# Performance work log

Hardware: AMD Instinct MI355X
Metric: run time of the kernel (lower is better)

The kernel has to match this reference:

```python
import jax, jax.numpy as jnp
import numpy as np

MAX_POINTS = 32
EPS = 1e-5


def setup_inputs() -> dict:
    key = jax.random.key(0)
    k1, k2, k3, k4, k5, k6 = jax.random.split(key, 6)
    M, P, C_IN, C_OUT = 40000, MAX_POINTS, 4, 64
    voxel_features = jax.random.normal(k1, (M, P, C_IN), dtype=jnp.float32)
    voxel_num_points = jax.random.randint(k2, (M,), 0, MAX_POINTS, dtype=jnp.int32)
    # Linear(C_in, C_out) params (PyTorch default init scale ~ U(-1/sqrt(fan_in), ...))
    lim = 1.0 / np.sqrt(C_IN)
    W = jax.random.uniform(k3, (C_OUT, C_IN), minval=-lim, maxval=lim, dtype=jnp.float32)
    b = jax.random.uniform(k4, (C_OUT,), minval=-lim, maxval=lim, dtype=jnp.float32)
    # BatchNorm1d affine params
    gamma = jnp.ones((C_OUT,), dtype=jnp.float32)
    beta = jnp.zeros((C_OUT,), dtype=jnp.float32)
    return {"voxel_features": voxel_features, "voxel_num_points": voxel_num_points,
            "W": W, "b": b, "gamma": gamma, "beta": beta}


def _vfe(x, n, W, b, gamma, beta):
    # x: (M, P, C_in), n: (M,) valid point counts
    mask = (jnp.arange(MAX_POINTS)[None, :] < n[:, None])            # (M, P)
    maskf = mask.astype(x.dtype)[..., None]                          # (M, P, 1)
    h = jnp.einsum('mpc,oc->mpo', x, W) + b                          # (M, P, C_out)
    h = h * maskf                                                    # zero invalid slots
    # BatchNorm1d (training-mode batch stats) over valid points only
    n_valid = jnp.maximum(jnp.sum(maskf), 1.0)
    mu = jnp.sum(h, axis=(0, 1)) / n_valid                           # (C_out,)
    d = (h - mu) * maskf
    var = jnp.sum(d * d, axis=(0, 1)) / n_valid                      # biased var, as BN
    hn = d * jax.lax.rsqrt(var + EPS) * gamma + beta * maskf
    hn = jax.nn.relu(hn) * maskf
    # per-voxel mean over valid points; voxels with n==0 output zeros
    counts = jnp.maximum(n.astype(x.dtype), 1.0)[:, None]
    return jnp.sum(hn, axis=1) / counts                              # (M, C_out)


def reference(voxel_features, voxel_num_points, W, b, gamma, beta):
    return _vfe(voxel_features, voxel_num_points, W, b, gamma, beta)
```

## Files before the change

kernel.cpp:

```cpp
#include <hip/hip_runtime.h>

#define MAX_POINTS 32
#define C_OUT 64
#define EPS 1e-5f

#define NMOM 15

__global__ __launch_bounds__(256) void vfe_stats(
    const float* __restrict__ x, const int* __restrict__ vnp,
    float* __restrict__ ws, int M)
{
    const int tid    = blockIdx.x * 256 + threadIdx.x;
    const int stride = gridDim.x * 256;
    const int total  = M * MAX_POINTS;

    float a[NMOM];
    #pragma unroll
    for (int i = 0; i < NMOM; ++i) a[i] = 0.f;

    const float4* __restrict__ xq = (const float4*)x;
    for (int i = tid; i < total; i += stride) {
        const int m = i >> 5;
        const int p = i & 31;
        const int n = vnp[m];
        const bool valid = p < n;
        float4 q = make_float4(0.f, 0.f, 0.f, 0.f);
        if (valid) q = xq[i];
        a[0] += q.x; a[1] += q.y; a[2] += q.z; a[3] += q.w;
        a[4]  = fmaf(q.x, q.x, a[4]);
        a[5]  = fmaf(q.x, q.y, a[5]);
        a[6]  = fmaf(q.x, q.z, a[6]);
        a[7]  = fmaf(q.x, q.w, a[7]);
        a[8]  = fmaf(q.y, q.y, a[8]);
        a[9]  = fmaf(q.y, q.z, a[9]);
        a[10] = fmaf(q.y, q.w, a[10]);
        a[11] = fmaf(q.z, q.z, a[11]);
        a[12] = fmaf(q.z, q.w, a[12]);
        a[13] = fmaf(q.w, q.w, a[13]);
        a[14] += valid ? 1.f : 0.f;
    }

    #pragma unroll
    for (int i = 0; i < NMOM; ++i) {
        float v = a[i];
        #pragma unroll
        for (int off = 32; off > 0; off >>= 1)
            v += __shfl_down(v, off, 64);
        a[i] = v;
    }

    __shared__ float bl[4][NMOM];
    const int lane = threadIdx.x & 63;
    const int wid  = threadIdx.x >> 6;
    if (lane == 0) {
        #pragma unroll
        for (int i = 0; i < NMOM; ++i) bl[wid][i] = a[i];
    }
    __syncthreads();
    if (threadIdx.x < NMOM) {
        const int i = threadIdx.x;
        atomicAdd(&ws[i], bl[0][i] + bl[1][i] + bl[2][i] + bl[3][i]);
    }
}

__global__ __launch_bounds__(256) void vfe_out(
    const float* __restrict__ x, const int* __restrict__ vnp,
    const float* __restrict__ W, const float* __restrict__ b,
    const float* __restrict__ gamma, const float* __restrict__ beta,
    const float* __restrict__ ws, float* __restrict__ out, int M)
{
    __shared__ float4 sx[32 * MAX_POINTS];
    const int lane = threadIdx.x & 63;
    const int wid  = threadIdx.x >> 6;

    const float4 w4  = ((const float4*)W)[lane];
    const float bias = b[lane];
    const float cnt  = ws[14];
    const float nv   = fmaxf(cnt, 1.0f);
    const float wdots = w4.x*ws[0] + w4.y*ws[1] + w4.z*ws[2] + w4.w*ws[3];
    const float S    = wdots + cnt * bias;
    const float mu   = S / nv;
    const float q2 = ws[4]*w4.x*w4.x + ws[8]*w4.y*w4.y + ws[11]*w4.z*w4.z + ws[13]*w4.w*w4.w
                   + 2.f*(ws[5]*w4.x*w4.y + ws[6]*w4.x*w4.z + ws[7]*w4.x*w4.w
                        + ws[9]*w4.y*w4.z + ws[10]*w4.y*w4.w + ws[12]*w4.z*w4.w);
    const float SS  = q2 + 2.f*bias*wdots + cnt*bias*bias;
    const float var = fmaxf(SS / nv - mu * mu, 0.f);
    const float A   = gamma[lane] * rsqrtf(var + EPS);
    const float B   = fmaf(-mu, A, beta[lane]);

    const int m0 = blockIdx.x * 32;

    const float4* __restrict__ xq = (const float4*)x + (size_t)m0 * MAX_POINTS;
    const int limit = min(1024, (M - m0) * MAX_POINTS);
    for (int t = threadIdx.x; t < limit; t += 256) sx[t] = xq[t];
    __syncthreads();

    #pragma unroll
    for (int v = 0; v < 8; ++v) {
        const int mv = wid * 8 + v;
        const int m  = m0 + mv;
        if (m >= M) break;
        const int n = vnp[m];
        const float4* __restrict__ q = &sx[mv * MAX_POINTS];
        float acc = 0.f;
        #pragma unroll 4
        for (int p = 0; p < n; ++p) {
            const float4 pt = q[p];
            const float h = fmaf(pt.x, w4.x, fmaf(pt.y, w4.y,
                            fmaf(pt.z, w4.z, fmaf(pt.w, w4.w, bias))));
            acc += fmaxf(fmaf(h, A, B), 0.f);
        }
        out[(size_t)m * C_OUT + lane] = acc / fmaxf((float)n, 1.0f);
    }
}

extern "C" void kernel_launch(void* const* d_in, const int* in_sizes, int n_in,
                              void* d_out, int out_size, void* d_ws, size_t ws_size,
                              hipStream_t stream) {
    const float* x     = (const float*)d_in[0];
    const int*   vnp   = (const int*)  d_in[1];
    const float* W     = (const float*)d_in[2];
    const float* b     = (const float*)d_in[3];
    const float* gamma = (const float*)d_in[4];
    const float* beta  = (const float*)d_in[5];
    float* out = (float*)d_out;
    float* ws  = (float*)d_ws;
    const int M = in_sizes[1];

    hipMemsetAsync(d_ws, 0, NMOM * sizeof(float), stream);
    vfe_stats<<<256, 256, 0, stream>>>(x, vnp, ws, M);
    const int nblk = (M + 31) / 32;
    vfe_out<<<nblk, 256, 0, stream>>>(x, vnp, W, b, gamma, beta, ws, out, M);
}
```

Baseline: 107.5 us.

## Fuse stats and output passes into one cooperative kernel with LDS-resident voxels

Replaces the memset plus two-kernel pipeline with a single cooperative kernel. Each block loads 157 voxels into shared memory once, accumulates the input moments, and writes per-block partials. After a grid-wide sync it reduces the partials and computes the output from the cached LDS data, so the input is read from global memory only once. This removes a launch, the memset and the global atomics. In exchange it needs all 255 blocks of 1024 threads with about 80KB of LDS each to be co-resident, and it pays the cost of a grid barrier.

```diff
diff --git a/kernel.cpp b/kernel.cpp
--- a/kernel.cpp
+++ b/kernel.cpp
@@ -1,31 +1,49 @@
 #include <hip/hip_runtime.h>
+#include <hip/hip_cooperative_groups.h>
+
+namespace cg = cooperative_groups;
 
 #define MAX_POINTS 32
 #define C_OUT 64
 #define EPS 1e-5f
 
 #define NMOM 15
+#define TPB 1024
+#define NWAVE (TPB / 64)
+#define VPB 157
 
-__global__ __launch_bounds__(256) void vfe_stats(
+__global__ __launch_bounds__(TPB) void vfe_fused(
     const float* __restrict__ x, const int* __restrict__ vnp,
-    float* __restrict__ ws, int M)
+    const float* __restrict__ W, const float* __restrict__ b,
+    const float* __restrict__ gamma, const float* __restrict__ beta,
+    float* __restrict__ wsp, float* __restrict__ out, int M)
 {
-    const int tid    = blockIdx.x * 256 + threadIdx.x;
-    const int stride = gridDim.x * 256;
-    const int total  = M * MAX_POINTS;
+    __shared__ float4 sx[VPB * MAX_POINTS];
+    __shared__ float  bl[NWAVE][NMOM];
+    __shared__ float  red[NMOM][16];
+    __shared__ float  smom[NMOM];
+
+    const int tid  = threadIdx.x;
+    const int lane = tid & 63;
+    const int wid  = tid >> 6;
+    const int base = blockIdx.x * VPB;
+    const int nvox = max(0, min(VPB, M - base));
+    const int slots = nvox * MAX_POINTS;
 
     float a[NMOM];
     #pragma unroll
     for (int i = 0; i < NMOM; ++i) a[i] = 0.f;
 
-    const float4* __restrict__ xq = (const float4*)x;
-    for (int i = tid; i < total; i += stride) {
-        const int m = i >> 5;
-        const int p = i & 31;
-        const int n = vnp[m];
-        const bool valid = p < n;
-        float4 q = make_float4(0.f, 0.f, 0.f, 0.f);
-        if (valid) q = xq[i];
+    const float4* __restrict__ xq = (const float4*)x + (size_t)base * MAX_POINTS;
+    for (int i = tid; i < slots; i += TPB) {
+        float4 q = xq[i];
+        sx[i] = q;
+        const int n = vnp[base + (i >> 5)];
+        if ((i & 31) < n) {
+            a[14] += 1.f;
+        } else {
+            q = make_float4(0.f, 0.f, 0.f, 0.f);
+        }
         a[0] += q.x; a[1] += q.y; a[2] += q.z; a[3] += q.w;
         a[4]  = fmaf(q.x, q.x, a[4]);
         a[5]  = fmaf(q.x, q.y, a[5]);
@@ -37,7 +55,6 @@
         a[11] = fmaf(q.z, q.z, a[11]);
         a[12] = fmaf(q.z, q.w, a[12]);
         a[13] = fmaf(q.w, q.w, a[13]);
-        a[14] += valid ? 1.f : 0.f;
     }
 
     #pragma unroll
@@ -48,58 +65,55 @@
             v += __shfl_down(v, off, 64);
         a[i] = v;
     }
-
-    __shared__ float bl[4][NMOM];
-    const int lane = threadIdx.x & 63;
-    const int wid  = threadIdx.x >> 6;
     if (lane == 0) {
         #pragma unroll
         for (int i = 0; i < NMOM; ++i) bl[wid][i] = a[i];
     }
     __syncthreads();
-    if (threadIdx.x < NMOM) {
-        const int i = threadIdx.x;
-        atomicAdd(&ws[i], bl[0][i] + bl[1][i] + bl[2][i] + bl[3][i]);
+    if (tid < NMOM) {
+        float s = 0.f;
+        #pragma unroll
+        for (int w = 0; w < NWAVE; ++w) s += bl[w][tid];
+        wsp[blockIdx.x * NMOM + tid] = s;
     }
-}
+    __threadfence();
+    cg::this_grid().sync();
 
-__global__ __launch_bounds__(256) void vfe_out(
-    const float* __restrict__ x, const int* __restrict__ vnp,
-    const float* __restrict__ W, const float* __restrict__ b,
-    const float* __restrict__ gamma, const float* __restrict__ beta,
-    const float* __restrict__ ws, float* __restrict__ out, int M)
-{
-    __shared__ float4 sx[32 * MAX_POINTS];
-    const int lane = threadIdx.x & 63;
-    const int wid  = threadIdx.x >> 6;
+    const int nb = gridDim.x;
+    if (tid < NMOM * 16) {
+        const int mom = tid >> 4;
+        const int g   = tid & 15;
+        float s = 0.f;
+        for (int bb = g; bb < nb; bb += 16) s += wsp[bb * NMOM + mom];
+        red[mom][g] = s;
+    }
+    __syncthreads();
+    if (tid < NMOM) {
+        float s = 0.f;
+        #pragma unroll
+        for (int g = 0; g < 16; ++g) s += red[tid][g];
+        smom[tid] = s;
+    }
+    __syncthreads();
 
     const float4 w4  = ((const float4*)W)[lane];
     const float bias = b[lane];
-    const float cnt  = ws[14];
+    const float cnt  = smom[14];
     const float nv   = fmaxf(cnt, 1.0f);
-    const float wdots = w4.x*ws[0] + w4.y*ws[1] + w4.z*ws[2] + w4.w*ws[3];
+    const float wdots = w4.x*smom[0] + w4.y*smom[1] + w4.z*smom[2] + w4.w*smom[3];
     const float S    = wdots + cnt * bias;
     const float mu   = S / nv;
-    const float q2 = ws[4]*w4.x*w4.x + ws[8]*w4.y*w4.y + ws[11]*w4.z*w4.z + ws[13]*w4.w*w4.w
-                   + 2.f*(ws[5]*w4.x*w4.y + ws[6]*w4.x*w4.z + ws[7]*w4.x*w4.w
-                        + ws[9]*w4.y*w4.z + ws[10]*w4.y*w4.w + ws[12]*w4.z*w4.w);
+    const float q2 = smom[4]*w4.x*w4.x + smom[8]*w4.y*w4.y + smom[11]*w4.z*w4.z
+                   + smom[13]*w4.w*w4.w
+                   + 2.f*(smom[5]*w4.x*w4.y + smom[6]*w4.x*w4.z + smom[7]*w4.x*w4.w
+                        + smom[9]*w4.y*w4.z + smom[10]*w4.y*w4.w + smom[12]*w4.z*w4.w);
     const float SS  = q2 + 2.f*bias*wdots + cnt*bias*bias;
     const float var = fmaxf(SS / nv - mu * mu, 0.f);
     const float A   = gamma[lane] * rsqrtf(var + EPS);
     const float B   = fmaf(-mu, A, beta[lane]);
 
-    const int m0 = blockIdx.x * 32;
-
-    const float4* __restrict__ xq = (const float4*)x + (size_t)m0 * MAX_POINTS;
-    const int limit = min(1024, (M - m0) * MAX_POINTS);
-    for (int t = threadIdx.x; t < limit; t += 256) sx[t] = xq[t];
-    __syncthreads();
-
-    #pragma unroll
-    for (int v = 0; v < 8; ++v) {
-        const int mv = wid * 8 + v;
-        const int m  = m0 + mv;
-        if (m >= M) break;
+    for (int mv = wid; mv < nvox; mv += NWAVE) {
+        const int m = base + mv;
         const int n = vnp[m];
         const float4* __restrict__ q = &sx[mv * MAX_POINTS];
         float acc = 0.f;
@@ -124,11 +138,12 @@
     const float* gamma = (const float*)d_in[4];
     const float* beta  = (const float*)d_in[5];
     float* out = (float*)d_out;
-    float* ws  = (float*)d_ws;
-    const int M = in_sizes[1];
+    float* wsp = (float*)d_ws;
+    int M = in_sizes[1];
 
-    hipMemsetAsync(d_ws, 0, NMOM * sizeof(float), stream);
-    vfe_stats<<<256, 256, 0, stream>>>(x, vnp, ws, M);
-    const int nblk = (M + 31) / 32;
-    vfe_out<<<nblk, 256, 0, stream>>>(x, vnp, W, b, gamma, beta, ws, out, M);
+    const int nblk = (M + VPB - 1) / VPB;
+    void* args[] = {(void*)&x, (void*)&vnp, (void*)&W, (void*)&b,
+                    (void*)&gamma, (void*)&beta, (void*)&wsp, (void*)&out, (void*)&M};
+    hipLaunchCooperativeKernel((void*)vfe_fused, dim3(nblk), dim3(TPB),
+                               args, 0, stream);
 }
```

Result: slower. 192.5 us (+79.1%).

## Replace atomic stats reduction with per-block partials and drop memset launch

Applied to the files above, without the earlier changes.

The stats kernel now writes per-block partial moments to a workspace array instead of atomically adding into global memory, which removes the memset launch and atomic contention. The output kernel reduces the 512 partials itself, and the prologue that loads its tile into shared memory overlaps with that reduction. The stats kernel launches with larger blocks and more of them, and loads x unconditionally so the loads are branch-free. The output kernel handles 64 voxels per 512-thread block. In exchange, every output block repeats the partial-sum reduction, and the unconditional loads read invalid point slots as well.

```diff
diff --git a/kernel.cpp b/kernel.cpp
--- a/kernel.cpp
+++ b/kernel.cpp
@@ -6,12 +6,20 @@
 
 #define NMOM 15
 
-__global__ __launch_bounds__(256) void vfe_stats(
+#define K1_BLOCKS 512
+#define K1_TPB 1024
+#define K1_NWAVE (K1_TPB / 64)
+
+#define K2_TPB 512
+#define K2_NWAVE (K2_TPB / 64)
+#define K2_VOX 64
+
+__global__ __launch_bounds__(K1_TPB) void vfe_stats(
     const float* __restrict__ x, const int* __restrict__ vnp,
-    float* __restrict__ ws, int M)
+    float* __restrict__ wsp, int M)
 {
-    const int tid    = blockIdx.x * 256 + threadIdx.x;
-    const int stride = gridDim.x * 256;
+    const int tid    = blockIdx.x * K1_TPB + threadIdx.x;
+    const int stride = K1_BLOCKS * K1_TPB;
     const int total  = M * MAX_POINTS;
 
     float a[NMOM];
@@ -20,12 +28,11 @@
 
     const float4* __restrict__ xq = (const float4*)x;
     for (int i = tid; i < total; i += stride) {
-        const int m = i >> 5;
-        const int p = i & 31;
-        const int n = vnp[m];
-        const bool valid = p < n;
-        float4 q = make_float4(0.f, 0.f, 0.f, 0.f);
-        if (valid) q = xq[i];
+        float4 q = xq[i];
+        const int n = vnp[i >> 5];
+        const bool valid = (i & 31) < n;
+        if (valid) a[14] += 1.f;
+        else       q = make_float4(0.f, 0.f, 0.f, 0.f);
         a[0] += q.x; a[1] += q.y; a[2] += q.z; a[3] += q.w;
         a[4]  = fmaf(q.x, q.x, a[4]);
         a[5]  = fmaf(q.x, q.y, a[5]);
@@ -37,7 +44,6 @@
         a[11] = fmaf(q.z, q.z, a[11]);
         a[12] = fmaf(q.z, q.w, a[12]);
         a[13] = fmaf(q.w, q.w, a[13]);
-        a[14] += valid ? 1.f : 0.f;
     }
 
     #pragma unroll
@@ -49,7 +55,7 @@
         a[i] = v;
     }
 
-    __shared__ float bl[4][NMOM];
+    __shared__ float bl[K1_NWAVE][NMOM];
     const int lane = threadIdx.x & 63;
     const int wid  = threadIdx.x >> 6;
     if (lane == 0) {
@@ -58,48 +64,61 @@
     }
     __syncthreads();
     if (threadIdx.x < NMOM) {
-        const int i = threadIdx.x;
-        atomicAdd(&ws[i], bl[0][i] + bl[1][i] + bl[2][i] + bl[3][i]);
+        float s = 0.f;
+        #pragma unroll
+        for (int w = 0; w < K1_NWAVE; ++w) s += bl[w][threadIdx.x];
+        wsp[threadIdx.x * K1_BLOCKS + blockIdx.x] = s;
     }
 }
 
-__global__ __launch_bounds__(256) void vfe_out(
+__global__ __launch_bounds__(K2_TPB) void vfe_out(
     const float* __restrict__ x, const int* __restrict__ vnp,
     const float* __restrict__ W, const float* __restrict__ b,
     const float* __restrict__ gamma, const float* __restrict__ beta,
-    const float* __restrict__ ws, float* __restrict__ out, int M)
+    const float* __restrict__ wsp, float* __restrict__ out, int M)
 {
-    __shared__ float4 sx[32 * MAX_POINTS];
+    __shared__ float4 sx[K2_VOX * MAX_POINTS];
+    __shared__ float  smom[NMOM];
+
     const int lane = threadIdx.x & 63;
     const int wid  = threadIdx.x >> 6;
+    const int m0   = blockIdx.x * K2_VOX;
+    const int nvox = max(0, min(K2_VOX, M - m0));
+
+    const float4* __restrict__ xq = (const float4*)x + (size_t)m0 * MAX_POINTS;
+    const int limit = nvox * MAX_POINTS;
+    for (int t = threadIdx.x; t < limit; t += K2_TPB) sx[t] = xq[t];
+
+    for (int mom = wid; mom < NMOM; mom += K2_NWAVE) {
+        const float4* __restrict__ pp = (const float4*)(wsp + mom * K1_BLOCKS);
+        const float4 v0 = pp[lane * 2];
+        const float4 v1 = pp[lane * 2 + 1];
+        float s = (v0.x + v0.y) + (v0.z + v0.w) + (v1.x + v1.y) + (v1.z + v1.w);
+        #pragma unroll
+        for (int off = 32; off > 0; off >>= 1)
+            s += __shfl_down(s, off, 64);
+        if (lane == 0) smom[mom] = s;
+    }
+    __syncthreads();
 
     const float4 w4  = ((const float4*)W)[lane];
     const float bias = b[lane];
-    const float cnt  = ws[14];
+    const float cnt  = smom[14];
     const float nv   = fmaxf(cnt, 1.0f);
-    const float wdots = w4.x*ws[0] + w4.y*ws[1] + w4.z*ws[2] + w4.w*ws[3];
+    const float wdots = w4.x*smom[0] + w4.y*smom[1] + w4.z*smom[2] + w4.w*smom[3];
     const float S    = wdots + cnt * bias;
     const float mu   = S / nv;
-    const float q2 = ws[4]*w4.x*w4.x + ws[8]*w4.y*w4.y + ws[11]*w4.z*w4.z + ws[13]*w4.w*w4.w
-                   + 2.f*(ws[5]*w4.x*w4.y + ws[6]*w4.x*w4.z + ws[7]*w4.x*w4.w
-                        + ws[9]*w4.y*w4.z + ws[10]*w4.y*w4.w + ws[12]*w4.z*w4.w);
+    const float q2 = smom[4]*w4.x*w4.x + smom[8]*w4.y*w4.y + smom[11]*w4.z*w4.z
+                   + smom[13]*w4.w*w4.w
+                   + 2.f*(smom[5]*w4.x*w4.y + smom[6]*w4.x*w4.z + smom[7]*w4.x*w4.w
+                        + smom[9]*w4.y*w4.z + smom[10]*w4.y*w4.w + smom[12]*w4.z*w4.w);
     const float SS  = q2 + 2.f*bias*wdots + cnt*bias*bias;
     const float var = fmaxf(SS / nv - mu * mu, 0.f);
     const float A   = gamma[lane] * rsqrtf(var + EPS);
     const float B   = fmaf(-mu, A, beta[lane]);
 
-    const int m0 = blockIdx.x * 32;
-
-    const float4* __restrict__ xq = (const float4*)x + (size_t)m0 * MAX_POINTS;
-    const int limit = min(1024, (M - m0) * MAX_POINTS);
-    for (int t = threadIdx.x; t < limit; t += 256) sx[t] = xq[t];
-    __syncthreads();
-
-    #pragma unroll
-    for (int v = 0; v < 8; ++v) {
-        const int mv = wid * 8 + v;
-        const int m  = m0 + mv;
-        if (m >= M) break;
+    for (int mv = wid; mv < nvox; mv += K2_NWAVE) {
+        const int m = m0 + mv;
         const int n = vnp[m];
         const float4* __restrict__ q = &sx[mv * MAX_POINTS];
         float acc = 0.f;
@@ -124,11 +143,10 @@
     const float* gamma = (const float*)d_in[4];
     const float* beta  = (const float*)d_in[5];
     float* out = (float*)d_out;
-    float* ws  = (float*)d_ws;
+    float* wsp = (float*)d_ws;
     const int M = in_sizes[1];
 
-    hipMemsetAsync(d_ws, 0, NMOM * sizeof(float), stream);
-    vfe_stats<<<256, 256, 0, stream>>>(x, vnp, ws, M);
-    const int nblk = (M + 31) / 32;
-    vfe_out<<<nblk, 256, 0, stream>>>(x, vnp, W, b, gamma, beta, ws, out, M);
+    vfe_stats<<<K1_BLOCKS, K1_TPB, 0, stream>>>(x, vnp, wsp, M);
+    const int nblk = (M + K2_VOX - 1) / K2_VOX;
+    vfe_out<<<nblk, K2_TPB, 0, stream>>>(x, vnp, W, b, gamma, beta, wsp, out, M);
 }
```

Measured after the change: 101.6 us. -5.5%, faster.
